# Optimization experiments

Hardware: AMD Instinct MI355X
Metric: run time of the kernel (lower is better)

## Reference

```python
import jax, jax.numpy as jnp
import numpy as np

K = 3        # num patches
S = 2        # scale factor
G = 32       # base glimpse size


def _avg_pool(x, k):
    # x: (b, c, H, W), kernel=stride=k (matches F.avg_pool2d(x, k))
    if k == 1:
        return x
    b, c, h, w = x.shape
    return x.reshape(b, c, h // k, k, w // k, k).mean(axis=(3, 5))


def _extract_patch(x, l, size):
    # x: (b, c, h, w); l: (b, 2) in [-1, 1]; returns (b, c, size, size)
    b, c, h, w = x.shape
    start = (0.5 * ((l + 1.0) * h)).astype(jnp.int32)  # (b, 2) [col, row]
    pad = size // 2 + 1
    xp = jnp.pad(x, ((0, 0), (0, 0), (pad, pad), (pad, pad)))

    def slice_one(img, st):
        # img: (c, hp, wp); st: (2,) -> rows use st[1], cols use st[0]
        return jax.lax.dynamic_slice(img, (0, st[1], st[0]), (c, size, size))

    return jax.vmap(slice_one)(xp, start)


def _foveate(x, l):
    phi = []
    size = G
    for _ in range(K):
        phi.append(_extract_patch(x, l, size))
        size = int(S * size)
    # pool every coarser patch back to GxG, concat on channel, flatten
    phi = [_avg_pool(p, p.shape[-1] // G) for p in phi]
    phi = jnp.concatenate(phi, axis=1)          # (b, K*c, G, G)
    return phi.reshape(phi.shape[0], -1)        # (b, K*c*G*G)


def setup_inputs() -> dict:
    key = jax.random.key(0)
    ks = jax.random.split(key, 10)
    b, c, h, w = 256, 3, 224, 224
    h_g = h_l = 1024
    dim = K * G * G * c  # 9216
    x = jax.random.normal(ks[0], (b, c, h, w), dtype=jnp.float32)
    l_prev = jax.random.uniform(ks[1], (b, 2), dtype=jnp.float32, minval=-1.0, maxval=1.0)
    def lin(k, fan_in, fan_out):
        return jax.random.normal(k, (fan_in, fan_out), dtype=jnp.float32) / np.sqrt(fan_in)
    return {
        "x": x, "l_prev": l_prev,
        "W1": lin(ks[2], dim, h_g), "b1": jnp.zeros((h_g,), jnp.float32),
        "W2": lin(ks[3], 2, h_l),   "b2": jnp.zeros((h_l,), jnp.float32),
        "W3": lin(ks[4], h_g, h_g + h_l), "b3": jnp.zeros((h_g + h_l,), jnp.float32),
        "W4": lin(ks[5], h_l, h_g + h_l), "b4": jnp.zeros((h_g + h_l,), jnp.float32),
    }


def reference(x, l_prev, W1, b1, W2, b2, W3, b3, W4, b4):
    glimpse = _foveate(x, l_prev)                       # (b, K*c*G*G)
    g_out = jax.nn.relu(glimpse @ W1 + b1)              # (b, h_g)
    l_out = jax.nn.relu(l_prev @ W2 + b2)               # (b, h_l)
    what = g_out @ W3 + b3                              # (b, h_g+h_l)
    where = l_out @ W4 + b4                             # (b, h_g+h_l)
    return jax.nn.relu(what + where)
```

## Files before the change

kernel.cpp:

```cpp
#include <hip/hip_runtime.h>

typedef __bf16 bf16_t;
typedef __bf16 bf16x8 __attribute__((ext_vector_type(8)));
typedef float f32x4 __attribute__((ext_vector_type(4)));
typedef unsigned short us4 __attribute__((ext_vector_type(4)));
typedef unsigned short us8 __attribute__((ext_vector_type(8)));

#define LO4(v) __builtin_shufflevector(v, v, 0, 1, 2, 3)
#define HI4(v) __builtin_shufflevector(v, v, 4, 5, 6, 7)

template<int F>
__device__ __forceinline__ void fov_scale(const float* __restrict__ xb,
                                          bf16_t* __restrict__ gb,
                                          int r0, int c0, int base, int count, int kidx)
{
  constexpr float inv = 1.0f / (F * F);
  for (int i = threadIdx.x; i < count; i += 256) {
    const int idx = base + i;
    const int ch  = idx >> 10;
    const int rem = idx & 1023;
    const int gy  = rem >> 5, gx = rem & 31;
    const float* xc = xb + ch * 50176;
    float sum = 0.0f;
    const int rbase = r0 + gy * F, cbase = c0 + gx * F;
#pragma unroll
    for (int dy = 0; dy < F; ++dy) {
      const int rr = rbase + dy;
      if ((unsigned)rr < 224u) {
#pragma unroll
        for (int dx = 0; dx < F; ++dx) {
          const int cc = cbase + dx;
          if ((unsigned)cc < 224u) sum += xc[rr * 224 + cc];
        }
      }
    }
    gb[kidx * 3072 + idx] = (bf16_t)(sum * inv);
  }
}

__device__ __forceinline__ void transpose_tile(const float* __restrict__ src, int srcld,
                                               unsigned short* __restrict__ dst, int dstld)
{
  __shared__ unsigned short T[64][72];
  const int t = threadIdx.x;
#pragma unroll
  for (int it = 0; it < 16; ++it) {
    const int idx = it * 256 + t;
    const int kk = idx >> 6, nn = idx & 63;
    T[nn][kk] = __builtin_bit_cast(unsigned short, (bf16_t)src[(size_t)kk * srcld + nn]);
  }
  __syncthreads();
#pragma unroll
  for (int it = 0; it < 2; ++it) {
    const int q = it * 256 + t;
    const int n = q >> 3, kc = (q & 7) * 8;
    *(us8*)(dst + (size_t)n * dstld + kc) = *(const us8*)&T[n][kc];
  }
}

__global__ __launch_bounds__(256) void fov_conv_kernel(const float* __restrict__ x,
                                                       const float* __restrict__ l,
                                                       bf16_t* __restrict__ g,
                                                       const float* __restrict__ W1,
                                                       const float* __restrict__ W3,
                                                       const float* __restrict__ W4,
                                                       bf16_t* __restrict__ W1t,
                                                       bf16_t* __restrict__ W34t)
{
  const int bid = blockIdx.x;
  if (bid < 1792) {
    const int b = bid & 255;
    const int y = bid >> 8;
    const float l0 = l[2 * b], l1 = l[2 * b + 1];
    const int st0 = (int)(0.5f * ((l0 + 1.0f) * 224.0f));
    const int st1 = (int)(0.5f * ((l1 + 1.0f) * 224.0f));
    const float* xb = x + (size_t)b * 3 * 50176;
    bf16_t* gb = g + (size_t)b * 9216;
    if (y == 0) {
      fov_scale<1>(xb, gb, st1 - 17, st0 - 17, 0, 3072, 0);
    } else if (y <= 2) {
      fov_scale<2>(xb, gb, st1 - 33, st0 - 33, (y - 1) * 1536, 1536, 1);
    } else {
      fov_scale<4>(xb, gb, st1 - 65, st0 - 65, (y - 3) * 768, 768, 2);
    }
  } else if (bid < 4096) {
    const int cid = bid - 1792;
    const int kt = cid >> 4, nt = cid & 15;
    transpose_tile(W1 + (size_t)(kt * 64) * 1024 + nt * 64, 1024,
                   (unsigned short*)W1t + (size_t)(nt * 64) * 9216 + kt * 64, 9216);
  } else {
    const int cid = bid - 4096;
    const int kt = cid >> 5, nt = cid & 31;
    const int k0 = kt * 64;
    const float* src = (k0 < 1024) ? (W3 + (size_t)k0 * 2048 + nt * 64)
                                   : (W4 + (size_t)(k0 - 1024) * 2048 + nt * 64);
    transpose_tile(src, 2048,
                   (unsigned short*)W34t + (size_t)(nt * 64) * 2048 + k0, 2048);
  }
}

template<int BM, int BN, int KCHUNK, int NDIM, int KFULL>
__global__ __launch_bounds__(256) void gemm_bb(const bf16_t* __restrict__ A,
                                               const bf16_t* __restrict__ Bt,
                                               float* __restrict__ part)
{
  constexpr int WROWS = BM / 4;
  constexpr int SM = WROWS / 16;
  constexpr int SN = BN / 16;
  constexpr int LDA = 36;
  constexpr int NLA = BM / 64;
  __shared__ unsigned short Al[BM * LDA];
  __shared__ unsigned short Bl[BN * LDA];
  const int t = threadIdx.x;
  const int w = t >> 6, lane = t & 63;
  const int lr = lane & 15, kg = lane >> 4;
  const int bm0 = blockIdx.x * BM, bn0 = blockIdx.y * BN;
  const int ks0 = blockIdx.z * KCHUNK;
  const unsigned short* Au = (const unsigned short*)A;
  const unsigned short* Bu = (const unsigned short*)Bt;

  const int bn = t >> 2, bkb = (t & 3) * 8;
  const bool bld = (t < BN * 4);

  f32x4 acc[SM][SN] = {};
  us8 pa[NLA], pb;

#pragma unroll
  for (int i = 0; i < NLA; ++i) {
    const int q = t + 256 * i;
    pa[i] = *(const us8*)(Au + (size_t)(bm0 + (q >> 2)) * KFULL + ks0 + (q & 3) * 8);
  }
  if (bld) pb = *(const us8*)(Bu + (size_t)(bn0 + bn) * KFULL + ks0 + bkb);

  for (int k0 = 0; k0 < KCHUNK; k0 += 32) {
#pragma unroll
    for (int i = 0; i < NLA; ++i) {
      const int q = t + 256 * i;
      const int m = q >> 2, kb = (q & 3) * 8;
      *(us4*)(&Al[m * LDA + kb])     = LO4(pa[i]);
      *(us4*)(&Al[m * LDA + kb + 4]) = HI4(pa[i]);
    }
    if (bld) {
      *(us4*)(&Bl[bn * LDA + bkb])     = LO4(pb);
      *(us4*)(&Bl[bn * LDA + bkb + 4]) = HI4(pb);
    }
    __syncthreads();
    if (k0 + 32 < KCHUNK) {
      const int knext = ks0 + k0 + 32;
#pragma unroll
      for (int i = 0; i < NLA; ++i) {
        const int q = t + 256 * i;
        pa[i] = *(const us8*)(Au + (size_t)(bm0 + (q >> 2)) * KFULL + knext + (q & 3) * 8);
      }
      if (bld) pb = *(const us8*)(Bu + (size_t)(bn0 + bn) * KFULL + knext + bkb);
    }
    bf16x8 af[SM], bfr[SN];
#pragma unroll
    for (int sm = 0; sm < SM; ++sm) {
      const unsigned short* p = &Al[(w * WROWS + sm * 16 + lr) * LDA + kg * 8];
      us4 x0 = *(const us4*)p;
      us4 x1 = *(const us4*)(p + 4);
      af[sm] = __builtin_bit_cast(bf16x8, __builtin_shufflevector(x0, x1, 0, 1, 2, 3, 4, 5, 6, 7));
    }
#pragma unroll
    for (int sn = 0; sn < SN; ++sn) {
      const unsigned short* p = &Bl[(sn * 16 + lr) * LDA + kg * 8];
      us4 x0 = *(const us4*)p;
      us4 x1 = *(const us4*)(p + 4);
      bfr[sn] = __builtin_bit_cast(bf16x8, __builtin_shufflevector(x0, x1, 0, 1, 2, 3, 4, 5, 6, 7));
    }
#pragma unroll
    for (int sm = 0; sm < SM; ++sm)
#pragma unroll
      for (int sn = 0; sn < SN; ++sn)
        acc[sm][sn] = __builtin_amdgcn_mfma_f32_16x16x32_bf16(af[sm], bfr[sn], acc[sm][sn], 0, 0, 0);
    __syncthreads();
  }
  float* outp = part + (size_t)blockIdx.z * ((size_t)256 * NDIM);
#pragma unroll
  for (int sm = 0; sm < SM; ++sm)
#pragma unroll
    for (int sn = 0; sn < SN; ++sn)
#pragma unroll
      for (int r = 0; r < 4; ++r) {
        const int gm = bm0 + w * WROWS + sm * 16 + kg * 4 + r;
        const int gn = bn0 + sn * 16 + lr;
        outp[(size_t)gm * NDIM + gn] = acc[sm][sn][r];
      }
}

__global__ __launch_bounds__(256) void fuse_mid(const float* __restrict__ part1,
                                                const float* __restrict__ b1,
                                                const float* __restrict__ lprev,
                                                const float* __restrict__ W2,
                                                const float* __restrict__ b2,
                                                bf16_t* __restrict__ A2)
{
  const int idx = blockIdx.x * 256 + threadIdx.x;
  const int row = idx >> 11, col = idx & 2047;
  float s;
  if (col < 1024) {
    s = b1[col];
#pragma unroll
    for (int i = 0; i < 16; ++i) s += part1[i * 262144 + row * 1024 + col];
  } else {
    const int n = col - 1024;
    s = fmaf(lprev[2 * row], W2[n], fmaf(lprev[2 * row + 1], W2[1024 + n], b2[n]));
  }
  A2[idx] = (bf16_t)fmaxf(s, 0.0f);
}

__global__ __launch_bounds__(256) void epilogue2(const float* __restrict__ part2,
                                                 const float* __restrict__ b3,
                                                 const float* __restrict__ b4,
                                                 float* __restrict__ out)
{
  const int idx = blockIdx.x * 256 + threadIdx.x;
  const int col = idx & 2047;
  float s = b3[col] + b4[col];
#pragma unroll
  for (int i = 0; i < 8; ++i) s += part2[i * 524288 + idx];
  out[idx] = fmaxf(s, 0.0f);
}

extern "C" void kernel_launch(void* const* d_in, const int* in_sizes, int n_in,
                              void* d_out, int out_size, void* d_ws, size_t ws_size,
                              hipStream_t stream)
{
  const float* x     = (const float*)d_in[0];
  const float* lprev = (const float*)d_in[1];
  const float* W1    = (const float*)d_in[2];
  const float* b1    = (const float*)d_in[3];
  const float* W2    = (const float*)d_in[4];
  const float* b2    = (const float*)d_in[5];
  const float* W3    = (const float*)d_in[6];
  const float* b3    = (const float*)d_in[7];
  const float* W4    = (const float*)d_in[8];
  const float* b4    = (const float*)d_in[9];
  float* out = (float*)d_out;

  char* ws = (char*)d_ws;
  bf16_t* glimpse = (bf16_t*)ws;
  bf16_t* A2      = (bf16_t*)(ws + 4718592);
  float*  part1   = (float*)(ws + 5767168);
  float*  part2   = (float*)(ws + 22544384);
  bf16_t* W1t     = (bf16_t*)(ws + 39321600);
  bf16_t* W34t    = (bf16_t*)(ws + 58195968);

  fov_conv_kernel<<<5120, 256, 0, stream>>>(x, lprev, glimpse, W1, W3, W4, W1t, W34t);
  gemm_bb<128, 64, 576, 1024, 9216>
      <<<dim3(2, 16, 16), 256, 0, stream>>>(glimpse, W1t, part1);
  fuse_mid<<<2048, 256, 0, stream>>>(part1, b1, lprev, W2, b2, A2);
  gemm_bb<128, 64, 256, 2048, 2048>
      <<<dim3(2, 32, 8), 256, 0, stream>>>(A2, W34t, part2);
  epilogue2<<<2048, 256, 0, stream>>>(part2, b3, b4, out);
}
```

Measured before the change: 287.5 us.

## Fuse all five stages into one cooperative persistent kernel with grid syncs

After: 782.7 us. +172.3%, slower.

```diff
diff --git a/kernel.cpp b/kernel.cpp
--- a/kernel.cpp
+++ b/kernel.cpp
@@ -1,4 +1,7 @@
 #include <hip/hip_runtime.h>
+#include <hip/hip_cooperative_groups.h>
+
+namespace cg = cooperative_groups;
 
 typedef __bf16 bf16_t;
 typedef __bf16 bf16x8 __attribute__((ext_vector_type(8)));
@@ -38,23 +41,220 @@
   }
 }
 
+__device__ __forceinline__ void fov_unit(const float* __restrict__ x,
+                                         const float* __restrict__ l,
+                                         bf16_t* __restrict__ g, int u)
+{
+  const int b = u & 255;
+  const int y = u >> 8;
+  const float l0 = l[2 * b], l1 = l[2 * b + 1];
+  const int st0 = (int)(0.5f * ((l0 + 1.0f) * 224.0f));
+  const int st1 = (int)(0.5f * ((l1 + 1.0f) * 224.0f));
+  const float* xb = x + (size_t)b * 3 * 50176;
+  bf16_t* gb = g + (size_t)b * 9216;
+  if (y == 0) {
+    fov_scale<1>(xb, gb, st1 - 17, st0 - 17, 0, 3072, 0);
+  } else if (y <= 2) {
+    fov_scale<2>(xb, gb, st1 - 33, st0 - 33, (y - 1) * 1536, 1536, 1);
+  } else {
+    fov_scale<4>(xb, gb, st1 - 65, st0 - 65, (y - 3) * 768, 768, 2);
+  }
+}
+
 __device__ __forceinline__ void transpose_tile(const float* __restrict__ src, int srcld,
-                                               unsigned short* __restrict__ dst, int dstld)
-{
-  __shared__ unsigned short T[64][72];
+                                               unsigned short* __restrict__ dst, int dstld,
+                                               unsigned short* __restrict__ T)
+{
   const int t = threadIdx.x;
+  __syncthreads();
 #pragma unroll
   for (int it = 0; it < 16; ++it) {
     const int idx = it * 256 + t;
     const int kk = idx >> 6, nn = idx & 63;
-    T[nn][kk] = __builtin_bit_cast(unsigned short, (bf16_t)src[(size_t)kk * srcld + nn]);
+    T[nn * 72 + kk] = __builtin_bit_cast(unsigned short, (bf16_t)src[(size_t)kk * srcld + nn]);
   }
   __syncthreads();
 #pragma unroll
   for (int it = 0; it < 2; ++it) {
     const int q = it * 256 + t;
     const int n = q >> 3, kc = (q & 7) * 8;
-    *(us8*)(dst + (size_t)n * dstld + kc) = *(const us8*)&T[n][kc];
+    *(us8*)(dst + (size_t)n * dstld + kc) = *(const us8*)&T[n * 72 + kc];
+  }
+}
+
+template<int BM, int BN, int KCHUNK, int NDIM, int KFULL>
+__device__ __forceinline__ void gemm_body(const bf16_t* __restrict__ A,
+                                          const bf16_t* __restrict__ Bt,
+                                          float* __restrict__ part,
+                                          int bx, int by, int bz,
+                                          unsigned short* __restrict__ sh)
+{
+  constexpr int WROWS = BM / 4;
+  constexpr int SM = WROWS / 16;
+  constexpr int SN = BN / 16;
+  constexpr int LDA = 36;
+  constexpr int NLA = BM / 64;
+  unsigned short* Al = sh;
+  unsigned short* Bl = sh + BM * LDA;
+  const int t = threadIdx.x;
+  const int w = t >> 6, lane = t & 63;
+  const int lr = lane & 15, kg = lane >> 4;
+  const int bm0 = bx * BM, bn0 = by * BN;
+  const int ks0 = bz * KCHUNK;
+  const unsigned short* Au = (const unsigned short*)A;
+  const unsigned short* Bu = (const unsigned short*)Bt;
+
+  const int bn = t >> 2, bkb = (t & 3) * 8;
+  const bool bld = (t < BN * 4);
+
+  f32x4 acc[SM][SN] = {};
+  us8 pa[NLA], pb;
+
+#pragma unroll
+  for (int i = 0; i < NLA; ++i) {
+    const int q = t + 256 * i;
+    pa[i] = *(const us8*)(Au + (size_t)(bm0 + (q >> 2)) * KFULL + ks0 + (q & 3) * 8);
+  }
+  if (bld) pb = *(const us8*)(Bu + (size_t)(bn0 + bn) * KFULL + ks0 + bkb);
+
+  for (int k0 = 0; k0 < KCHUNK; k0 += 32) {
+#pragma unroll
+    for (int i = 0; i < NLA; ++i) {
+      const int q = t + 256 * i;
+      const int m = q >> 2, kb = (q & 3) * 8;
+      *(us4*)(&Al[m * LDA + kb])     = LO4(pa[i]);
+      *(us4*)(&Al[m * LDA + kb + 4]) = HI4(pa[i]);
+    }
+    if (bld) {
+      *(us4*)(&Bl[bn * LDA + bkb])     = LO4(pb);
+      *(us4*)(&Bl[bn * LDA + bkb + 4]) = HI4(pb);
+    }
+    __syncthreads();
+    if (k0 + 32 < KCHUNK) {
+      const int knext = ks0 + k0 + 32;
+#pragma unroll
+      for (int i = 0; i < NLA; ++i) {
+        const int q = t + 256 * i;
+        pa[i] = *(const us8*)(Au + (size_t)(bm0 + (q >> 2)) * KFULL + knext + (q & 3) * 8);
+      }
+      if (bld) pb = *(const us8*)(Bu + (size_t)(bn0 + bn) * KFULL + knext + bkb);
+    }
+    bf16x8 af[SM], bfr[SN];
+#pragma unroll
+    for (int sm = 0; sm < SM; ++sm) {
+      const unsigned short* p = &Al[(w * WROWS + sm * 16 + lr) * LDA + kg * 8];
+      us4 x0 = *(const us4*)p;
+      us4 x1 = *(const us4*)(p + 4);
+      af[sm] = __builtin_bit_cast(bf16x8, __builtin_shufflevector(x0, x1, 0, 1, 2, 3, 4, 5, 6, 7));
+    }
+#pragma unroll
+    for (int sn = 0; sn < SN; ++sn) {
+      const unsigned short* p = &Bl[(sn * 16 + lr) * LDA + kg * 8];
+      us4 x0 = *(const us4*)p;
+      us4 x1 = *(const us4*)(p + 4);
+      bfr[sn] = __builtin_bit_cast(bf16x8, __builtin_shufflevector(x0, x1, 0, 1, 2, 3, 4, 5, 6, 7));
+    }
+#pragma unroll
+    for (int sm = 0; sm < SM; ++sm)
+#pragma unroll
+      for (int sn = 0; sn < SN; ++sn)
+        acc[sm][sn] = __builtin_amdgcn_mfma_f32_16x16x32_bf16(af[sm], bfr[sn], acc[sm][sn], 0, 0, 0);
+    __syncthreads();
+  }
+  float* outp = part + (size_t)bz * ((size_t)256 * NDIM);
+#pragma unroll
+  for (int sm = 0; sm < SM; ++sm)
+#pragma unroll
+    for (int sn = 0; sn < SN; ++sn)
+#pragma unroll
+      for (int r = 0; r < 4; ++r) {
+        const int gm = bm0 + w * WROWS + sm * 16 + kg * 4 + r;
+        const int gn = bn0 + sn * 16 + lr;
+        outp[(size_t)gm * NDIM + gn] = acc[sm][sn][r];
+      }
+}
+
+__global__ __launch_bounds__(256, 2) void mega(const float* __restrict__ x,
+                                               const float* __restrict__ lprev,
+                                               const float* __restrict__ W1,
+                                               const float* __restrict__ b1,
+                                               const float* __restrict__ W2,
+                                               const float* __restrict__ b2,
+                                               const float* __restrict__ W3,
+                                               const float* __restrict__ b3,
+                                               const float* __restrict__ W4,
+                                               const float* __restrict__ b4,
+                                               bf16_t* __restrict__ glimpse,
+                                               bf16_t* __restrict__ A2,
+                                               float* __restrict__ part1,
+                                               float* __restrict__ part2,
+                                               bf16_t* __restrict__ W1t,
+                                               bf16_t* __restrict__ W34t,
+                                               float* __restrict__ out)
+{
+  __shared__ unsigned short sh[(128 + 64) * 36];
+  const int t = threadIdx.x;
+  cg::grid_group grid = cg::this_grid();
+
+  for (int u = blockIdx.x; u < 5120; u += 512) {
+    if (u < 1792) {
+      fov_unit(x, lprev, glimpse, u);
+    } else if (u < 4096) {
+      const int cid = u - 1792;
+      const int kt = cid >> 4, nt = cid & 15;
+      transpose_tile(W1 + (size_t)(kt * 64) * 1024 + nt * 64, 1024,
+                     (unsigned short*)W1t + (size_t)(nt * 64) * 9216 + kt * 64, 9216, sh);
+    } else {
+      const int cid = u - 4096;
+      const int kt = cid >> 5, nt = cid & 31;
+      const int k0 = kt * 64;
+      const float* src = (k0 < 1024) ? (W3 + (size_t)k0 * 2048 + nt * 64)
+                                     : (W4 + (size_t)(k0 - 1024) * 2048 + nt * 64);
+      transpose_tile(src, 2048,
+                     (unsigned short*)W34t + (size_t)(nt * 64) * 2048 + k0, 2048, sh);
+    }
+  }
+  __threadfence();
+  grid.sync();
+
+  {
+    const int u = blockIdx.x;
+    gemm_body<128, 64, 576, 1024, 9216>(glimpse, W1t, part1, u & 1, (u >> 1) & 15, u >> 5, sh);
+  }
+  __threadfence();
+  grid.sync();
+
+  for (int blk = blockIdx.x; blk < 2048; blk += 512) {
+    const int idx = blk * 256 + t;
+    const int row = idx >> 11, col = idx & 2047;
+    float s;
+    if (col < 1024) {
+      s = b1[col];
+#pragma unroll
+      for (int i = 0; i < 16; ++i) s += part1[i * 262144 + row * 1024 + col];
+    } else {
+      const int n = col - 1024;
+      s = fmaf(lprev[2 * row], W2[n], fmaf(lprev[2 * row + 1], W2[1024 + n], b2[n]));
+    }
+    A2[idx] = (bf16_t)fmaxf(s, 0.0f);
+  }
+  __threadfence();
+  grid.sync();
+
+  {
+    const int u = blockIdx.x;
+    gemm_body<128, 64, 256, 2048, 2048>(A2, W34t, part2, u & 1, (u >> 1) & 31, u >> 6, sh);
+  }
+  __threadfence();
+  grid.sync();
+
+  for (int blk = blockIdx.x; blk < 2048; blk += 512) {
+    const int idx = blk * 256 + t;
+    const int col = idx & 2047;
+    float s = b3[col] + b4[col];
+#pragma unroll
+    for (int i = 0; i < 8; ++i) s += part2[i * 524288 + idx];
+    out[idx] = fmaxf(s, 0.0f);
   }
 }
 
@@ -67,27 +267,15 @@
                                                        bf16_t* __restrict__ W1t,
                                                        bf16_t* __restrict__ W34t)
 {
+  __shared__ unsigned short T[64 * 72];
   const int bid = blockIdx.x;
   if (bid < 1792) {
-    const int b = bid & 255;
-    const int y = bid >> 8;
-    const float l0 = l[2 * b], l1 = l[2 * b + 1];
-    const int st0 = (int)(0.5f * ((l0 + 1.0f) * 224.0f));
-    const int st1 = (int)(0.5f * ((l1 + 1.0f) * 224.0f));
-    const float* xb = x + (size_t)b * 3 * 50176;
-    bf16_t* gb = g + (size_t)b * 9216;
-    if (y == 0) {
-      fov_scale<1>(xb, gb, st1 - 17, st0 - 17, 0, 3072, 0);
-    } else if (y <= 2) {
-      fov_scale<2>(xb, gb, st1 - 33, st0 - 33, (y - 1) * 1536, 1536, 1);
-    } else {
-      fov_scale<4>(xb, gb, st1 - 65, st0 - 65, (y - 3) * 768, 768, 2);
-    }
+    fov_unit(x, l, g, bid);
   } else if (bid < 4096) {
     const int cid = bid - 1792;
     const int kt = cid >> 4, nt = cid & 15;
     transpose_tile(W1 + (size_t)(kt * 64) * 1024 + nt * 64, 1024,
-                   (unsigned short*)W1t + (size_t)(nt * 64) * 9216 + kt * 64, 9216);
+                   (unsigned short*)W1t + (size_t)(nt * 64) * 9216 + kt * 64, 9216, T);
   } else {
     const int cid = bid - 4096;
     const int kt = cid >> 5, nt = cid & 31;
@@ -95,7 +283,7 @@
     const float* src = (k0 < 1024) ? (W3 + (size_t)k0 * 2048 + nt * 64)
                                    : (W4 + (size_t)(k0 - 1024) * 2048 + nt * 64);
     transpose_tile(src, 2048,
-                   (unsigned short*)W34t + (size_t)(nt * 64) * 2048 + k0, 2048);
+                   (unsigned short*)W34t + (size_t)(nt * 64) * 2048 + k0, 2048, T);
   }
 }
 
@@ -104,89 +292,8 @@
                                                const bf16_t* __restrict__ Bt,
                                                float* __restrict__ part)
 {
-  constexpr int WROWS = BM / 4;
-  constexpr int SM = WROWS / 16;
-  constexpr int SN = BN / 16;
-  constexpr int LDA = 36;
-  constexpr int NLA = BM / 64;
-  __shared__ unsigned short Al[BM * LDA];
-  __shared__ unsigned short Bl[BN * LDA];
-  const int t = threadIdx.x;
-  const int w = t >> 6, lane = t & 63;
-  const int lr = lane & 15, kg = lane >> 4;
-  const int bm0 = blockIdx.x * BM, bn0 = blockIdx.y * BN;
-  const int ks0 = blockIdx.z * KCHUNK;
-  const unsigned short* Au = (const unsigned short*)A;
-  const unsigned short* Bu = (const unsigned short*)Bt;
-
-  const int bn = t >> 2, bkb = (t & 3) * 8;
-  const bool bld = (t < BN * 4);
-
-  f32x4 acc[SM][SN] = {};
-  us8 pa[NLA], pb;
-
-#pragma unroll
-  for (int i = 0; i < NLA; ++i) {
-    const int q = t + 256 * i;
-    pa[i] = *(const us8*)(Au + (size_t)(bm0 + (q >> 2)) * KFULL + ks0 + (q & 3) * 8);
-  }
-  if (bld) pb = *(const us8*)(Bu + (size_t)(bn0 + bn) * KFULL + ks0 + bkb);
-
-  for (int k0 = 0; k0 < KCHUNK; k0 += 32) {
-#pragma unroll
-    for (int i = 0; i < NLA; ++i) {
-      const int q = t + 256 * i;
-      const int m = q >> 2, kb = (q & 3) * 8;
-      *(us4*)(&Al[m * LDA + kb])     = LO4(pa[i]);
-      *(us4*)(&Al[m * LDA + kb + 4]) = HI4(pa[i]);
-    }
-    if (bld) {
-      *(us4*)(&Bl[bn * LDA + bkb])     = LO4(pb);
-      *(us4*)(&Bl[bn * LDA + bkb + 4]) = HI4(pb);
-    }
-    __syncthreads();
-    if (k0 + 32 < KCHUNK) {
-      const int knext = ks0 + k0 + 32;
-#pragma unroll
-      for (int i = 0; i < NLA; ++i) {
-        const int q = t + 256 * i;
-        pa[i] = *(const us8*)(Au + (size_t)(bm0 + (q >> 2)) * KFULL + knext + (q & 3) * 8);
-      }
-      if (bld) pb = *(const us8*)(Bu + (size_t)(bn0 + bn) * KFULL + knext + bkb);
-    }
-    bf16x8 af[SM], bfr[SN];
-#pragma unroll
-    for (int sm = 0; sm < SM; ++sm) {
-      const unsigned short* p = &Al[(w * WROWS + sm * 16 + lr) * LDA + kg * 8];
-      us4 x0 = *(const us4*)p;
-      us4 x1 = *(const us4*)(p + 4);
-      af[sm] = __builtin_bit_cast(bf16x8, __builtin_shufflevector(x0, x1, 0, 1, 2, 3, 4, 5, 6, 7));
-    }
-#pragma unroll
-    for (int sn = 0; sn < SN; ++sn) {
-      const unsigned short* p = &Bl[(sn * 16 + lr) * LDA + kg * 8];
-      us4 x0 = *(const us4*)p;
-      us4 x1 = *(const us4*)(p + 4);
-      bfr[sn] = __builtin_bit_cast(bf16x8, __builtin_shufflevector(x0, x1, 0, 1, 2, 3, 4, 5, 6, 7));
-    }
-#pragma unroll
-    for (int sm = 0; sm < SM; ++sm)
-#pragma unroll
-      for (int sn = 0; sn < SN; ++sn)
-        acc[sm][sn] = __builtin_amdgcn_mfma_f32_16x16x32_bf16(af[sm], bfr[sn], acc[sm][sn], 0, 0, 0);
-    __syncthreads();
-  }
-  float* outp = part + (size_t)blockIdx.z * ((size_t)256 * NDIM);
-#pragma unroll
-  for (int sm = 0; sm < SM; ++sm)
-#pragma unroll
-    for (int sn = 0; sn < SN; ++sn)
-#pragma unroll
-      for (int r = 0; r < 4; ++r) {
-        const int gm = bm0 + w * WROWS + sm * 16 + kg * 4 + r;
-        const int gn = bn0 + sn * 16 + lr;
-        outp[(size_t)gm * NDIM + gn] = acc[sm][sn][r];
-      }
+  __shared__ unsigned short sh[(BM + BN) * 36];
+  gemm_body<BM, BN, KCHUNK, NDIM, KFULL>(A, Bt, part, blockIdx.x, blockIdx.y, blockIdx.z, sh);
 }
 
 __global__ __launch_bounds__(256) void fuse_mid(const float* __restrict__ part1,
@@ -247,11 +354,31 @@
   bf16_t* W1t     = (bf16_t*)(ws + 39321600);
   bf16_t* W34t    = (bf16_t*)(ws + 58195968);
 
-  fov_conv_kernel<<<5120, 256, 0, stream>>>(x, lprev, glimpse, W1, W3, W4, W1t, W34t);
-  gemm_bb<128, 64, 576, 1024, 9216>
-      <<<dim3(2, 16, 16), 256, 0, stream>>>(glimpse, W1t, part1);
-  fuse_mid<<<2048, 256, 0, stream>>>(part1, b1, lprev, W2, b2, A2);
-  gemm_bb<128, 64, 256, 2048, 2048>
-      <<<dim3(2, 32, 8), 256, 0, stream>>>(A2, W34t, part2);
-  epilogue2<<<2048, 256, 0, stream>>>(part2, b3, b4, out);
-}
+  static int coop_blocks_per_cu = -1;
+  if (coop_blocks_per_cu < 0) {
+    int n = 0;
+    if (hipOccupancyMaxActiveBlocksPerMultiprocessor(&n, (const void*)mega, 256, 0) != hipSuccess)
+      n = 0;
+    coop_blocks_per_cu = n;
+  }
+
+  bool coop_done = false;
+  if (coop_blocks_per_cu >= 2) {
+    void* args[] = { (void*)&x, (void*)&lprev, (void*)&W1, (void*)&b1, (void*)&W2, (void*)&b2,
+                     (void*)&W3, (void*)&b3, (void*)&W4, (void*)&b4,
+                     (void*)&glimpse, (void*)&A2, (void*)&part1, (void*)&part2,
+                     (void*)&W1t, (void*)&W34t, (void*)&out };
+    coop_done = (hipLaunchCooperativeKernel((const void*)mega, dim3(512), dim3(256),
+                                            args, 0, stream) == hipSuccess);
+  }
+
+  if (!coop_done) {
+    fov_conv_kernel<<<5120, 256, 0, stream>>>(x, lprev, glimpse, W1, W3, W4, W1t, W34t);
+    gemm_bb<128, 64, 576, 1024, 9216>
+        <<<dim3(2, 16, 16), 256, 0, stream>>>(glimpse, W1t, part1);
+    fuse_mid<<<2048, 256, 0, stream>>>(part1, b1, lprev, W2, b2, A2);
+    gemm_bb<128, 64, 256, 2048, 2048>
+        <<<dim3(2, 32, 8), 256, 0, stream>>>(A2, W34t, part2);
+    epilogue2<<<2048, 256, 0, stream>>>(part2, b3, b4, out);
+  }
+}
```

## Fuse split-K reductions into GEMM kernels via atomic last-block counters

Applied to the files above, without the earlier changes.

Measured after the change: 605.6 us. 2.11x slower.

```diff
diff --git a/kernel.cpp b/kernel.cpp
--- a/kernel.cpp
+++ b/kernel.cpp
@@ -38,23 +38,43 @@
   }
 }
 
+__device__ __forceinline__ void fov_unit(const float* __restrict__ x,
+                                         const float* __restrict__ l,
+                                         bf16_t* __restrict__ g, int u)
+{
+  const int b = u & 255;
+  const int y = u >> 8;
+  const float l0 = l[2 * b], l1 = l[2 * b + 1];
+  const int st0 = (int)(0.5f * ((l0 + 1.0f) * 224.0f));
+  const int st1 = (int)(0.5f * ((l1 + 1.0f) * 224.0f));
+  const float* xb = x + (size_t)b * 3 * 50176;
+  bf16_t* gb = g + (size_t)b * 9216;
+  if (y == 0) {
+    fov_scale<1>(xb, gb, st1 - 17, st0 - 17, 0, 3072, 0);
+  } else if (y <= 2) {
+    fov_scale<2>(xb, gb, st1 - 33, st0 - 33, (y - 1) * 1536, 1536, 1);
+  } else {
+    fov_scale<4>(xb, gb, st1 - 65, st0 - 65, (y - 3) * 768, 768, 2);
+  }
+}
+
 __device__ __forceinline__ void transpose_tile(const float* __restrict__ src, int srcld,
-                                               unsigned short* __restrict__ dst, int dstld)
-{
-  __shared__ unsigned short T[64][72];
+                                               unsigned short* __restrict__ dst, int dstld,
+                                               unsigned short* __restrict__ T)
+{
   const int t = threadIdx.x;
 #pragma unroll
   for (int it = 0; it < 16; ++it) {
     const int idx = it * 256 + t;
     const int kk = idx >> 6, nn = idx & 63;
-    T[nn][kk] = __builtin_bit_cast(unsigned short, (bf16_t)src[(size_t)kk * srcld + nn]);
+    T[nn * 72 + kk] = __builtin_bit_cast(unsigned short, (bf16_t)src[(size_t)kk * srcld + nn]);
   }
   __syncthreads();
 #pragma unroll
   for (int it = 0; it < 2; ++it) {
     const int q = it * 256 + t;
     const int n = q >> 3, kc = (q & 7) * 8;
-    *(us8*)(dst + (size_t)n * dstld + kc) = *(const us8*)&T[n][kc];
+    *(us8*)(dst + (size_t)n * dstld + kc) = *(const us8*)&T[n * 72 + kc];
   }
 }
 
@@ -65,29 +85,19 @@
                                                        const float* __restrict__ W3,
                                                        const float* __restrict__ W4,
                                                        bf16_t* __restrict__ W1t,
-                                                       bf16_t* __restrict__ W34t)
-{
+                                                       bf16_t* __restrict__ W34t,
+                                                       int* __restrict__ ctrs)
+{
+  __shared__ unsigned short T[64 * 72];
   const int bid = blockIdx.x;
+  if (bid == 0 && threadIdx.x < 96) ctrs[threadIdx.x] = 0;
   if (bid < 1792) {
-    const int b = bid & 255;
-    const int y = bid >> 8;
-    const float l0 = l[2 * b], l1 = l[2 * b + 1];
-    const int st0 = (int)(0.5f * ((l0 + 1.0f) * 224.0f));
-    const int st1 = (int)(0.5f * ((l1 + 1.0f) * 224.0f));
-    const float* xb = x + (size_t)b * 3 * 50176;
-    bf16_t* gb = g + (size_t)b * 9216;
-    if (y == 0) {
-      fov_scale<1>(xb, gb, st1 - 17, st0 - 17, 0, 3072, 0);
-    } else if (y <= 2) {
-      fov_scale<2>(xb, gb, st1 - 33, st0 - 33, (y - 1) * 1536, 1536, 1);
-    } else {
-      fov_scale<4>(xb, gb, st1 - 65, st0 - 65, (y - 3) * 768, 768, 2);
-    }
+    fov_unit(x, l, g, bid);
   } else if (bid < 4096) {
     const int cid = bid - 1792;
     const int kt = cid >> 4, nt = cid & 15;
     transpose_tile(W1 + (size_t)(kt * 64) * 1024 + nt * 64, 1024,
-                   (unsigned short*)W1t + (size_t)(nt * 64) * 9216 + kt * 64, 9216);
+                   (unsigned short*)W1t + (size_t)(nt * 64) * 9216 + kt * 64, 9216, T);
   } else {
     const int cid = bid - 4096;
     const int kt = cid >> 5, nt = cid & 31;
@@ -95,27 +105,29 @@
     const float* src = (k0 < 1024) ? (W3 + (size_t)k0 * 2048 + nt * 64)
                                    : (W4 + (size_t)(k0 - 1024) * 2048 + nt * 64);
     transpose_tile(src, 2048,
-                   (unsigned short*)W34t + (size_t)(nt * 64) * 2048 + k0, 2048);
+                   (unsigned short*)W34t + (size_t)(nt * 64) * 2048 + k0, 2048, T);
   }
 }
 
 template<int BM, int BN, int KCHUNK, int NDIM, int KFULL>
-__global__ __launch_bounds__(256) void gemm_bb(const bf16_t* __restrict__ A,
-                                               const bf16_t* __restrict__ Bt,
-                                               float* __restrict__ part)
+__device__ __forceinline__ void gemm_body(const bf16_t* __restrict__ A,
+                                          const bf16_t* __restrict__ Bt,
+                                          float* __restrict__ part,
+                                          int bx, int by, int bz,
+                                          unsigned short* __restrict__ sh)
 {
   constexpr int WROWS = BM / 4;
   constexpr int SM = WROWS / 16;
   constexpr int SN = BN / 16;
   constexpr int LDA = 36;
   constexpr int NLA = BM / 64;
-  __shared__ unsigned short Al[BM * LDA];
-  __shared__ unsigned short Bl[BN * LDA];
+  unsigned short* Al = sh;
+  unsigned short* Bl = sh + BM * LDA;
   const int t = threadIdx.x;
   const int w = t >> 6, lane = t & 63;
   const int lr = lane & 15, kg = lane >> 4;
-  const int bm0 = blockIdx.x * BM, bn0 = blockIdx.y * BN;
-  const int ks0 = blockIdx.z * KCHUNK;
+  const int bm0 = bx * BM, bn0 = by * BN;
+  const int ks0 = bz * KCHUNK;
   const unsigned short* Au = (const unsigned short*)A;
   const unsigned short* Bu = (const unsigned short*)Bt;
 
@@ -176,7 +188,7 @@
         acc[sm][sn] = __builtin_amdgcn_mfma_f32_16x16x32_bf16(af[sm], bfr[sn], acc[sm][sn], 0, 0, 0);
     __syncthreads();
   }
-  float* outp = part + (size_t)blockIdx.z * ((size_t)256 * NDIM);
+  float* outp = part + (size_t)bz * ((size_t)256 * NDIM);
 #pragma unroll
   for (int sm = 0; sm < SM; ++sm)
 #pragma unroll
@@ -189,38 +201,59 @@
       }
 }
 
-__global__ __launch_bounds__(256) void fuse_mid(const float* __restrict__ part1,
-                                                const float* __restrict__ b1,
-                                                const float* __restrict__ lprev,
-                                                const float* __restrict__ W2,
-                                                const float* __restrict__ b2,
-                                                bf16_t* __restrict__ A2)
-{
-  const int idx = blockIdx.x * 256 + threadIdx.x;
-  const int row = idx >> 11, col = idx & 2047;
-  float s;
-  if (col < 1024) {
-    s = b1[col];
-#pragma unroll
-    for (int i = 0; i < 16; ++i) s += part1[i * 262144 + row * 1024 + col];
-  } else {
-    const int n = col - 1024;
-    s = fmaf(lprev[2 * row], W2[n], fmaf(lprev[2 * row + 1], W2[1024 + n], b2[n]));
-  }
-  A2[idx] = (bf16_t)fmaxf(s, 0.0f);
-}
-
-__global__ __launch_bounds__(256) void epilogue2(const float* __restrict__ part2,
-                                                 const float* __restrict__ b3,
-                                                 const float* __restrict__ b4,
-                                                 float* __restrict__ out)
-{
-  const int idx = blockIdx.x * 256 + threadIdx.x;
-  const int col = idx & 2047;
-  float s = b3[col] + b4[col];
-#pragma unroll
-  for (int i = 0; i < 8; ++i) s += part2[i * 524288 + idx];
-  out[idx] = fmaxf(s, 0.0f);
+template<int BM, int BN, int KCHUNK, int NDIM, int KFULL, int NZ, int EPI>
+__global__ __launch_bounds__(256) void gemm_fused(const bf16_t* __restrict__ A,
+                                                  const bf16_t* __restrict__ Bt,
+                                                  float* __restrict__ part,
+                                                  const float* __restrict__ bias0,
+                                                  const float* __restrict__ bias1,
+                                                  const float* __restrict__ lprev,
+                                                  const float* __restrict__ W2,
+                                                  void* __restrict__ dst,
+                                                  int* __restrict__ ctr)
+{
+  const int bx = blockIdx.x, by = blockIdx.y, bz = blockIdx.z;
+  const int t = threadIdx.x;
+
+  if (EPI == 1 && by == NDIM / BN) {
+    if (bz != 0) return;
+#pragma unroll 4
+    for (int e = 0; e < BM * 1024 / 256; ++e) {
+      const int lin = e * 256 + t;
+      const int row = bx * BM + (lin >> 10), col = lin & 1023;
+      const float s = fmaf(lprev[2 * row], W2[col],
+                      fmaf(lprev[2 * row + 1], W2[1024 + col], bias1[col]));
+      ((bf16_t*)dst)[(size_t)row * 2048 + 1024 + col] = (bf16_t)fmaxf(s, 0.0f);
+    }
+    return;
+  }
+
+  __shared__ unsigned short sh[(BM + BN) * 36];
+  __shared__ int lastflag;
+  gemm_body<BM, BN, KCHUNK, NDIM, KFULL>(A, Bt, part, bx, by, bz, sh);
+
+  __threadfence();
+  __syncthreads();
+  if (t == 0)
+    lastflag = (atomicAdd(&ctr[by * 2 + bx], 1) == NZ - 1);
+  __syncthreads();
+  if (!lastflag) return;
+  __threadfence();
+
+  const int bm0 = bx * BM, bn0 = by * BN;
+#pragma unroll
+  for (int e = 0; e < BM * BN / 256; ++e) {
+    const int lin = e * 256 + t;
+    const int r = lin >> 6, c = lin & (BN - 1);
+    const int gm = bm0 + r, gn = bn0 + c;
+    float s = (EPI == 1) ? bias0[gn] : bias0[gn] + bias1[gn];
+    const volatile float* p = part + (size_t)gm * NDIM + gn;
+#pragma unroll
+    for (int z = 0; z < NZ; ++z) s += p[(size_t)z * 256 * NDIM];
+    s = fmaxf(s, 0.0f);
+    if (EPI == 1) ((bf16_t*)dst)[(size_t)gm * 2048 + gn] = (bf16_t)s;
+    else          ((float*)dst)[(size_t)gm * 2048 + gn] = s;
+  }
 }
 
 extern "C" void kernel_launch(void* const* d_in, const int* in_sizes, int n_in,
@@ -246,12 +279,11 @@
   float*  part2   = (float*)(ws + 22544384);
   bf16_t* W1t     = (bf16_t*)(ws + 39321600);
   bf16_t* W34t    = (bf16_t*)(ws + 58195968);
-
-  fov_conv_kernel<<<5120, 256, 0, stream>>>(x, lprev, glimpse, W1, W3, W4, W1t, W34t);
-  gemm_bb<128, 64, 576, 1024, 9216>
-      <<<dim3(2, 16, 16), 256, 0, stream>>>(glimpse, W1t, part1);
-  fuse_mid<<<2048, 256, 0, stream>>>(part1, b1, lprev, W2, b2, A2);
-  gemm_bb<128, 64, 256, 2048, 2048>
-      <<<dim3(2, 32, 8), 256, 0, stream>>>(A2, W34t, part2);
-  epilogue2<<<2048, 256, 0, stream>>>(part2, b3, b4, out);
-}
+  int*    ctrs    = (int*)(ws + 66584576);
+
+  fov_conv_kernel<<<5120, 256, 0, stream>>>(x, lprev, glimpse, W1, W3, W4, W1t, W34t, ctrs);
+  gemm_fused<128, 64, 576, 1024, 9216, 16, 1>
+      <<<dim3(2, 17, 16), 256, 0, stream>>>(glimpse, W1t, part1, b1, b2, lprev, W2, A2, ctrs);
+  gemm_fused<128, 64, 256, 2048, 2048, 8, 2>
+      <<<dim3(2, 32, 8), 256, 0, stream>>>(A2, W34t, part2, b3, b4, nullptr, nullptr, out, ctrs + 32);
+}
```
